# Performance work log

Measured on AMD Instinct MI355X. Metric: run time of the kernel, lower is better.

## Reference

```python
import jax, jax.numpy as jnp
import numpy as np

TAU = 0.7
N_NODES = 1024
N_EDGES = 32768

def _mlp3(x, W1, b1, W2, b2, W3, b3):
    h = jax.nn.relu(x @ W1 + b1)
    h = jax.nn.relu(h @ W2 + b2)
    return h @ W3 + b3

def _gcn_conv(x, src, dst, W, b, n):
    # PyG GCNConv(add_self_loops=False): out = D^-1/2 A D^-1/2 (x W) + b
    deg = jax.ops.segment_sum(jnp.ones(src.shape[0], x.dtype), dst, num_segments=n)
    dinv = jnp.where(deg > 0, jax.lax.rsqrt(jnp.maximum(deg, 1.0)), 0.0)
    h = x @ W
    msg = h[src] * (dinv[src] * dinv[dst])[:, None]
    return jax.ops.segment_sum(msg, dst, num_segments=n) + b

def _forward(x1, x11, x2, mlp_W1, mlp_b1, mlp_W2, mlp_b2, mlp_W3, mlp_b3,
             m1_W1, m1_b1, m1_W2, m1_b2, m1_W3, m1_b3,
             wm1, bp1, bp2, wm12, wm13, class2,
             gcn1_W, gcn1_b, wm2, gcn2_W, gcn2_b, fc_W, fc_b, src, dst):
    n = x1.shape[0]
    logits = _mlp3(x1, mlp_W1, mlp_b1, mlp_W2, mlp_b2, mlp_W3, mlp_b3)  # [N,3]
    g = _mlp3(x11, m1_W1, m1_b1, m1_W2, m1_b2, m1_W3, m1_b3)            # [N,2]
    # hard argmax routing, softened: tau at argmax, (1-tau)/2 at the 2 others
    oh = jax.nn.one_hot(jnp.argmax(logits, axis=1), 3, dtype=logits.dtype)
    r = oh * TAU + (1.0 - oh) * ((1.0 - TAU) * 0.5)                     # [N,3]
    # fused form of: (einsum('nj,jkl',g,class2) * x2[...,None]).sum(-1) + g@b1
    res1 = jnp.einsum('nj,jkl,nk->nk', g, class2, x2) + g @ bp1         # [N,768]
    # fused form of: (einsum('nj,jkl',r,wm1) * res1[...,None]).sum(-1) + r@b2
    res1 = jnp.einsum('nj,jkl,nk->nk', r, wm1, res1) + r @ bp2          # [N,768]
    h1 = jax.nn.relu(_gcn_conv(res1, src, dst, gcn1_W, gcn1_b, n))      # [N,256]
    h1 = (r @ wm12) * h1 + 2e-4 * (res1 @ wm13)                         # [N,256]
    res2 = jnp.einsum('nj,jkl,nk->nk', r, wm2, h1)                      # [N,256]
    h2 = jax.nn.relu(_gcn_conv(res2, src, dst, gcn2_W, gcn2_b, n))      # [N,32]
    return jax.nn.log_softmax(h2 @ fc_W + fc_b, axis=1)                 # [N,8]

def setup_inputs():
    key = jax.random.key(0)
    ks = jax.random.split(key, 32)
    f = jnp.float32
    nrm = lambda i, s, sc=0.05: sc * jax.random.normal(ks[i], s, f)
    return {
        'x1': nrm(0, (N_NODES, 768), 1.0),
        'x11': nrm(1, (N_NODES, 768), 1.0),
        'x2': nrm(2, (N_NODES, 768), 1.0),
        'mlp_W1': nrm(3, (768, 512)), 'mlp_b1': jnp.zeros((512,), f),
        'mlp_W2': nrm(4, (512, 512)), 'mlp_b2': jnp.zeros((512,), f),
        'mlp_W3': nrm(5, (512, 3)), 'mlp_b3': jnp.zeros((3,), f),
        'm1_W1': nrm(6, (768, 512)), 'm1_b1': jnp.zeros((512,), f),
        'm1_W2': nrm(7, (512, 512)), 'm1_b2': jnp.zeros((512,), f),
        'm1_W3': nrm(8, (512, 2)), 'm1_b3': jnp.zeros((2,), f),
        'wm1': nrm(9, (3, 768, 256)),
        'bp1': jnp.zeros((2, 768), f),
        'bp2': jnp.zeros((3, 768), f),
        'wm12': jnp.ones((3, 256), f),
        'wm13': nrm(10, (768, 256)),
        'class2': jnp.ones((2, 768, 64), f),
        'gcn1_W': nrm(11, (768, 256)), 'gcn1_b': jnp.zeros((256,), f),
        'wm2': nrm(12, (3, 256, 256)),
        'gcn2_W': nrm(13, (256, 32)), 'gcn2_b': jnp.zeros((32,), f),
        'fc_W': nrm(14, (32, 8)), 'fc_b': jnp.zeros((8,), f),
        'edge_index': jax.random.randint(ks[15], (2, N_EDGES), 0, N_NODES),
    }

def reference(x1, x11, x2, mlp_W1, mlp_b1, mlp_W2, mlp_b2, mlp_W3, mlp_b3,
              m1_W1, m1_b1, m1_W2, m1_b2, m1_W3, m1_b3,
              wm1, bp1, bp2, wm12, wm13, class2,
              gcn1_W, gcn1_b, wm2, gcn2_W, gcn2_b, fc_W, fc_b, edge_index):
    src, dst = edge_index[0], edge_index[1]
    return _forward(x1, x11, x2, mlp_W1, mlp_b1, mlp_W2, mlp_b2, mlp_W3, mlp_b3,
                    m1_W1, m1_b1, m1_W2, m1_b2, m1_W3, m1_b3,
                    wm1, bp1, bp2, wm12, wm13, class2,
                    gcn1_W, gcn1_b, wm2, gcn2_W, gcn2_b, fc_W, fc_b, src, dst)
```

## Files before the change

### kernel.cpp

```cpp
#include <hip/hip_runtime.h>
#include <hip/hip_bf16.h>

#define NN 1024
#define NE 32768
#define TAU 0.7f
#define GAPT 0.01f

typedef __attribute__((ext_vector_type(8))) short short8;
typedef __attribute__((ext_vector_type(4))) float f32x4;

__device__ inline ushort bf16rne(float x) {
    union { float f; unsigned u; } a; a.f = x;
    unsigned r = (a.u + 0x7FFFu + ((a.u >> 16) & 1u)) >> 16;
    return (ushort)r;
}
__device__ inline float bf16tof(ushort h) {
    union { unsigned u; float f; } a; a.u = ((unsigned)h) << 16;
    return a.f;
}
__device__ inline void bf16split(float x, ushort& h, ushort& l) {
    h = bf16rne(x);
    l = bf16rne(x - bf16tof(h));
}

template <int K, int EPI>
__device__ __forceinline__ void gemm_wave(
    int lane, int rt, int ct,
    const ushort* __restrict__ Ah, const ushort* __restrict__ Al,
    const ushort* __restrict__ Bh, const ushort* __restrict__ Bl,
    const float* __restrict__ bias, const float* __restrict__ W3,
    float* __restrict__ Cf, ushort* __restrict__ Oh, ushort* __restrict__ Ol, int N) {
    int r0 = rt * 16, c0 = ct * 32;
    int g = lane >> 4, q = lane & 15;
    const ushort* pah = Ah + (size_t)(r0 + q) * K + g * 8;
    const ushort* pal = Al + (size_t)(r0 + q) * K + g * 8;
    const ushort* pb0h = Bh + (size_t)(c0 + q) * K + g * 8;
    const ushort* pb0l = Bl + (size_t)(c0 + q) * K + g * 8;
    const ushort* pb1h = pb0h + (size_t)16 * K;
    const ushort* pb1l = pb0l + (size_t)16 * K;
    f32x4 acc0 = {0.f, 0.f, 0.f, 0.f};
    f32x4 acc1 = {0.f, 0.f, 0.f, 0.f};
#pragma unroll 2
    for (int k0 = 0; k0 < K; k0 += 32) {
        short8 ah = *(const short8*)(pah + k0);
        short8 al = *(const short8*)(pal + k0);
        short8 b0h = *(const short8*)(pb0h + k0);
        short8 b0l = *(const short8*)(pb0l + k0);
        short8 b1h = *(const short8*)(pb1h + k0);
        short8 b1l = *(const short8*)(pb1l + k0);
        acc0 = __builtin_amdgcn_mfma_f32_16x16x32_bf16(ah, b0h, acc0, 0, 0, 0);
        acc1 = __builtin_amdgcn_mfma_f32_16x16x32_bf16(ah, b1h, acc1, 0, 0, 0);
        acc0 = __builtin_amdgcn_mfma_f32_16x16x32_bf16(ah, b0l, acc0, 0, 0, 0);
        acc1 = __builtin_amdgcn_mfma_f32_16x16x32_bf16(ah, b1l, acc1, 0, 0, 0);
        acc0 = __builtin_amdgcn_mfma_f32_16x16x32_bf16(al, b0h, acc0, 0, 0, 0);
        acc1 = __builtin_amdgcn_mfma_f32_16x16x32_bf16(al, b1h, acc1, 0, 0, 0);
    }
    int col0 = c0 + q, col1 = c0 + 16 + q;
    if constexpr (EPI == 0) {
#pragma unroll
        for (int i = 0; i < 4; i++) {
            int row = r0 + g * 4 + i;
            Cf[(size_t)row * N + col0] = acc0[i];
            Cf[(size_t)row * N + col1] = acc1[i];
        }
    } else if constexpr (EPI == 1) {
        float bv0 = bias[col0], bv1 = bias[col1];
#pragma unroll
        for (int i = 0; i < 4; i++) {
            int row = r0 + g * 4 + i;
            float a0 = fmaxf(acc0[i] + bv0, 0.f);
            float a1 = fmaxf(acc1[i] + bv1, 0.f);
            ushort h, l;
            bf16split(a0, h, l);
            Oh[(size_t)row * N + col0] = h;
            Ol[(size_t)row * N + col0] = l;
            bf16split(a1, h, l);
            Oh[(size_t)row * N + col1] = h;
            Ol[(size_t)row * N + col1] = l;
        }
    } else {
        constexpr int J = (EPI == 2) ? 3 : 2;
        constexpr int STR = (EPI == 2) ? 4 : 2;
        float bv0 = bias[col0], bv1 = bias[col1];
        float s[4][J];
#pragma unroll
        for (int i = 0; i < 4; i++) {
            float a0 = fmaxf(acc0[i] + bv0, 0.f);
            float a1 = fmaxf(acc1[i] + bv1, 0.f);
#pragma unroll
            for (int j = 0; j < J; j++)
                s[i][j] = a0 * W3[col0 * J + j] + a1 * W3[col1 * J + j];
        }
#pragma unroll
        for (int i = 0; i < 4; i++)
#pragma unroll
            for (int j = 0; j < J; j++) {
                float v = s[i][j];
#pragma unroll
                for (int m = 1; m < 16; m <<= 1) v += __shfl_xor(v, m);
                s[i][j] = v;
            }
        if (q == 0) {
#pragma unroll
            for (int i = 0; i < 4; i++) {
                int row = r0 + g * 4 + i;
#pragma unroll
                for (int j = 0; j < J; j++) atomicAdd(&Cf[(size_t)row * STR + j], s[i][j]);
            }
        }
    }
}

template <int M, int N, int K, int EPI>
__global__ __launch_bounds__(256) void gemm3(
    const ushort* __restrict__ Ah, const ushort* __restrict__ Al,
    const ushort* __restrict__ Bh, const ushort* __restrict__ Bl,
    float* __restrict__ Cf) {
    constexpr int RT = M / 16;
    constexpr int JOBS = RT * (N / 32);
    int wid = (blockIdx.x * 256 + threadIdx.x) >> 6;
    if (wid >= JOBS) return;
    gemm_wave<K, EPI>(threadIdx.x & 63, wid % RT, wid / RT, Ah, Al, Bh, Bl,
                      nullptr, nullptr, Cf, nullptr, nullptr, N);
}

template <int K, int EPI0, int EPI1, int RIDER>
__global__ __launch_bounds__(256) void gemm_pair(
    const ushort* __restrict__ Ah0, const ushort* __restrict__ Al0,
    const ushort* __restrict__ Bh0, const ushort* __restrict__ Bl0,
    const float* __restrict__ bias0, const float* __restrict__ W30,
    float* __restrict__ Cf0, ushort* __restrict__ Oh0, ushort* __restrict__ Ol0,
    const ushort* __restrict__ Ah1, const ushort* __restrict__ Al1,
    const ushort* __restrict__ Bh1, const ushort* __restrict__ Bl1,
    const float* __restrict__ bias1, const float* __restrict__ W31,
    float* __restrict__ Cf1, ushort* __restrict__ Oh1, ushort* __restrict__ Ol1,
    const int* __restrict__ esrc, const int* __restrict__ edst,
    const int* __restrict__ deg, int* __restrict__ rowst, int* __restrict__ cursor,
    float* __restrict__ dinv, int* __restrict__ adj) {
    if (RIDER == 1 && blockIdx.x >= 512) {
        __shared__ int ps[256];
        int t = threadIdx.x;
        int4 d4 = *(const int4*)(deg + t * 4);
        int sum = d4.x + d4.y + d4.z + d4.w;
        ps[t] = sum;
        __syncthreads();
        for (int off = 1; off < 256; off <<= 1) {
            int v = (t >= off) ? ps[t - off] : 0;
            __syncthreads();
            ps[t] += v;
            __syncthreads();
        }
        int r0 = ps[t] - sum;
        int r1 = r0 + d4.x, r2 = r1 + d4.y, r3 = r2 + d4.z;
        rowst[t * 4 + 0] = r0;
        rowst[t * 4 + 1] = r1;
        rowst[t * 4 + 2] = r2;
        rowst[t * 4 + 3] = r3;
        if (t == 255) rowst[1024] = r3 + d4.w;
        cursor[t * 4 + 0] = r0;
        cursor[t * 4 + 1] = r1;
        cursor[t * 4 + 2] = r2;
        cursor[t * 4 + 3] = r3;
        dinv[t * 4 + 0] = d4.x > 0 ? rsqrtf((float)d4.x) : 0.f;
        dinv[t * 4 + 1] = d4.y > 0 ? rsqrtf((float)d4.y) : 0.f;
        dinv[t * 4 + 2] = d4.z > 0 ? rsqrtf((float)d4.z) : 0.f;
        dinv[t * 4 + 3] = d4.w > 0 ? rsqrtf((float)d4.w) : 0.f;
        return;
    }
    if (RIDER == 2 && blockIdx.x >= 512) {
        int e = (blockIdx.x - 512) * 256 + threadIdx.x;
        int d = edst[e];
        int slot = atomicAdd(&cursor[d], 1);
        adj[slot] = esrc[e];
        return;
    }
    int wid = (blockIdx.x * 256 + threadIdx.x) >> 6;
    int lane = threadIdx.x & 63;
    int pair = wid >> 10;
    int widl = wid & 1023;
    int rt = widl & 63, ct = widl >> 6;
    if (pair == 0)
        gemm_wave<K, EPI0>(lane, rt, ct, Ah0, Al0, Bh0, Bl0, bias0, W30, Cf0, Oh0, Ol0, 512);
    else
        gemm_wave<K, EPI1>(lane, rt, ct, Ah1, Al1, Bh1, Bl1, bias1, W31, Cf1, Oh1, Ol1, 512);
}

__device__ void dev_zero(int sub, int t, float* zbase) {
    for (int i = sub * 256 + t; i < 6144; i += 512) zbase[i] = 0.f;
}

__device__ void dev_tabs_wave(int gw, int lane, const float* __restrict__ class2,
                              const float* __restrict__ wm1, const float* __restrict__ wm2,
                              float* __restrict__ C2s, float* __restrict__ Wm1s,
                              float* __restrict__ Wm2s) {
    if (gw < 2304) {
        float4 v = *(const float4*)(wm1 + (size_t)gw * 256 + lane * 4);
        float s = v.x + v.y + v.z + v.w;
#pragma unroll
        for (int m = 32; m; m >>= 1) s += __shfl_xor(s, m);
        if (lane == 0) Wm1s[gw] = s;
    } else if (gw < 3072) {
        int j = gw - 2304;
        float4 v = *(const float4*)(wm2 + (size_t)j * 256 + lane * 4);
        float s = v.x + v.y + v.z + v.w;
#pragma unroll
        for (int m = 32; m; m >>= 1) s += __shfl_xor(s, m);
        if (lane == 0) Wm2s[j] = s;
    } else {
        int row = (gw - 3072) * 4 + (lane >> 4);
        float4 v = *(const float4*)(class2 + (size_t)row * 64 + (lane & 15) * 4);
        float s = v.x + v.y + v.z + v.w;
#pragma unroll
        for (int m = 8; m; m >>= 1) s += __shfl_xor(s, m);
        if ((lane & 15) == 0) C2s[row] = s;
    }
}

__device__ void dev_splitx(int sub, int t, const float* __restrict__ X,
                           ushort* __restrict__ Xh, ushort* __restrict__ Xl) {
    int j = sub * 256 + t;
    float4 v = ((const float4*)X)[j];
    ushort h0, l0, h1, l1, h2, l2, h3, l3;
    bf16split(v.x, h0, l0);
    bf16split(v.y, h1, l1);
    bf16split(v.z, h2, l2);
    bf16split(v.w, h3, l3);
    ((ushort4*)Xh)[j] = make_ushort4(h0, h1, h2, h3);
    ((ushort4*)Xl)[j] = make_ushort4(l0, l1, l2, l3);
}

__global__ __launch_bounds__(1024) void aux0(
    const float* class2, const float* wm1, const float* wm2,
    float* C2s, float* Wm1s, float* Wm2s, float* zbase,
    const float* x1, ushort* XH1, ushort* XL1,
    const float* x11, ushort* XH2, ushort* XL2,
    const float* W1a, ushort* W1AH, ushort* W1AL,
    const float* W1b, ushort* W1BH, ushort* W1BL,
    const float* W2a, ushort* W2AH, ushort* W2AL,
    const float* W2b, ushort* W2BH, ushort* W2BL,
    const float* G1W, ushort* GWH, ushort* GWL,
    const float* W13, const int* edst, int* deg) {
    __shared__ float tb[4][32][33];
    int quad = threadIdx.x >> 8;
    int t = threadIdx.x & 255;
    int sub = blockIdx.x * 4 + quad;
    if (sub >= 4194) return;
    const float* W = nullptr;
    ushort *Th = nullptr, *Tl = nullptr;
    int K = 0, N = 0, tile = 0;
    if (sub >= 4066) {
        int e = (sub - 4066) * 256 + t;
        atomicAdd(&deg[edst[e]], 1);
    }
    else if (sub >= 3874) { W = W13; Th = GWH + 256 * 768; Tl = GWL + 256 * 768; K = 768; N = 256; tile = sub - 3874; }
    else if (sub >= 3682) { W = G1W; Th = GWH; Tl = GWL; K = 768; N = 256; tile = sub - 3682; }
    else if (sub >= 3426) { W = W2b; Th = W2BH; Tl = W2BL; K = 512; N = 512; tile = sub - 3426; }
    else if (sub >= 3170) { W = W2a; Th = W2AH; Tl = W2AL; K = 512; N = 512; tile = sub - 3170; }
    else if (sub >= 2786) { W = W1b; Th = W1BH; Tl = W1BL; K = 768; N = 512; tile = sub - 2786; }
    else if (sub >= 2402) { W = W1a; Th = W1AH; Tl = W1AL; K = 768; N = 512; tile = sub - 2402; }
    int k0 = 0, n0 = 0;
    if (W) {
        k0 = (tile % (K / 32)) * 32;
        n0 = (tile / (K / 32)) * 32;
        int tx = t % 32, ty = t / 32;
        for (int i = ty; i < 32; i += 8)
            tb[quad][i][tx] = W[(size_t)(k0 + i) * N + n0 + tx];
    } else if (sub < 2) dev_zero(sub, t, zbase);
    else if (sub < 866) dev_tabs_wave((sub - 2) * 4 + (t >> 6), t & 63,
                                      class2, wm1, wm2, C2s, Wm1s, Wm2s);
    else if (sub < 1634) dev_splitx(sub - 866, t, x1, XH1, XL1);
    else if (sub < 2402) dev_splitx(sub - 1634, t, x11, XH2, XL2);
    __syncthreads();
    if (W) {
        int tx = t % 32, ty = t / 32;
        for (int i = ty; i < 32; i += 8) {
            float v = tb[quad][tx][i];
            ushort h, l;
            bf16split(v, h, l);
            Th[(size_t)(n0 + i) * K + k0 + tx] = h;
            Tl[(size_t)(n0 + i) * K + k0 + tx] = l;
        }
    }
}

__global__ __launch_bounds__(256) void finrep(
    const float* __restrict__ LG, const float* __restrict__ b3, float* __restrict__ rbuf,
    const float* __restrict__ x1, const float* __restrict__ W1, const float* __restrict__ b1,
    const float* __restrict__ W2, const float* __restrict__ b2, const float* __restrict__ W3) {
    __shared__ int snode[4];
    __shared__ int scnt;
    __shared__ float part[4][512];
    __shared__ float xs[768];
    __shared__ float h1[512];
    __shared__ float h2[512];
    int t = threadIdx.x;
    if (t == 0) scnt = 0;
    __syncthreads();
    if (t < 4) {
        int n = blockIdx.x * 4 + t;
        float l0 = LG[n * 4 + 0] + b3[0];
        float l1 = LG[n * 4 + 1] + b3[1];
        float l2 = LG[n * 4 + 2] + b3[2];
        int am = 0;
        float mv = l0;
        if (l1 > mv) { mv = l1; am = 1; }
        if (l2 > mv) { mv = l2; am = 2; }
        float sec = (am == 0) ? fmaxf(l1, l2) : ((am == 1) ? fmaxf(l0, l2) : fmaxf(l0, l1));
        float lo = (1.f - TAU) * 0.5f;
        rbuf[n * 4 + 0] = (am == 0) ? TAU : lo;
        rbuf[n * 4 + 1] = (am == 1) ? TAU : lo;
        rbuf[n * 4 + 2] = (am == 2) ? TAU : lo;
        if (mv - sec < GAPT) {
            int s = atomicAdd(&scnt, 1);
            snode[s] = n;
        }
    }
    __syncthreads();
    int cnt = scnt;
    int w = t >> 6, l = t & 63;
    for (int it = 0; it < cnt; it++) {
        int n = snode[it];
        for (int k = t; k < 768; k += 256) xs[k] = x1[(size_t)n * 768 + k];
        __syncthreads();
        {
            float acc[8] = {0.f, 0.f, 0.f, 0.f, 0.f, 0.f, 0.f, 0.f};
            for (int k = w * 192; k < (w + 1) * 192; k++) {
                float xv = xs[k];
                const float* wr = W1 + (size_t)k * 512 + l;
#pragma unroll
                for (int c = 0; c < 8; c++) acc[c] += xv * wr[64 * c];
            }
#pragma unroll
            for (int c = 0; c < 8; c++) part[w][l + 64 * c] = acc[c];
        }
        __syncthreads();
        for (int d = t; d < 512; d += 256)
            h1[d] = fmaxf(part[0][d] + part[1][d] + part[2][d] + part[3][d] + b1[d], 0.f);
        __syncthreads();
        {
            float acc[8] = {0.f, 0.f, 0.f, 0.f, 0.f, 0.f, 0.f, 0.f};
            for (int k = w * 128; k < (w + 1) * 128; k++) {
                float xv = h1[k];
                const float* wr = W2 + (size_t)k * 512 + l;
#pragma unroll
                for (int c = 0; c < 8; c++) acc[c] += xv * wr[64 * c];
            }
#pragma unroll
            for (int c = 0; c < 8; c++) part[w][l + 64 * c] = acc[c];
        }
        __syncthreads();
        for (int d = t; d < 512; d += 256)
            h2[d] = fmaxf(part[0][d] + part[1][d] + part[2][d] + part[3][d] + b2[d], 0.f);
        __syncthreads();
        if (t < 64) {
            float p0 = 0.f, p1 = 0.f, p2 = 0.f;
            for (int k = t; k < 512; k += 64) {
                float hv = h2[k];
                p0 += hv * W3[k * 3 + 0];
                p1 += hv * W3[k * 3 + 1];
                p2 += hv * W3[k * 3 + 2];
            }
            for (int off = 32; off; off >>= 1) {
                p0 += __shfl_down(p0, off);
                p1 += __shfl_down(p1, off);
                p2 += __shfl_down(p2, off);
            }
            if (t == 0) {
                float l0 = p0 + b3[0], l1 = p1 + b3[1], l2 = p2 + b3[2];
                int am = 0;
                float mv = l0;
                if (l1 > mv) { mv = l1; am = 1; }
                if (l2 > mv) { mv = l2; am = 2; }
                float lo = (1.f - TAU) * 0.5f;
                rbuf[n * 4 + 0] = (am == 0) ? TAU : lo;
                rbuf[n * 4 + 1] = (am == 1) ? TAU : lo;
                rbuf[n * 4 + 2] = (am == 2) ? TAU : lo;
            }
        }
        __syncthreads();
    }
}

__global__ __launch_bounds__(256) void res1_kernel(
    const float* __restrict__ x2, const float* __restrict__ G, const float* __restrict__ m1b3,
    const float* __restrict__ rbuf, const float* __restrict__ C2s, const float* __restrict__ bp1,
    const float* __restrict__ Wm1s, const float* __restrict__ bp2,
    ushort* __restrict__ r1h, ushort* __restrict__ r1l) {
    int idx = blockIdx.x * 256 + threadIdx.x;
    int n = idx / 192;
    int kq = (idx % 192) * 4;
    float g0 = G[n * 2 + 0] + m1b3[0], g1 = G[n * 2 + 1] + m1b3[1];
    float r0 = rbuf[n * 4 + 0], r1 = rbuf[n * 4 + 1], r2 = rbuf[n * 4 + 2];
    float4 xv = *(const float4*)(x2 + (size_t)n * 768 + kq);
    float4 c0 = *(const float4*)(C2s + kq);
    float4 c1 = *(const float4*)(C2s + 768 + kq);
    float4 p0 = *(const float4*)(bp1 + kq);
    float4 p1 = *(const float4*)(bp1 + 768 + kq);
    float4 w0 = *(const float4*)(Wm1s + kq);
    float4 w1 = *(const float4*)(Wm1s + 768 + kq);
    float4 w2 = *(const float4*)(Wm1s + 1536 + kq);
    float4 q0 = *(const float4*)(bp2 + kq);
    float4 q1 = *(const float4*)(bp2 + 768 + kq);
    float4 q2 = *(const float4*)(bp2 + 1536 + kq);
    float o[4];
    o[0] = (xv.x * (g0 * c0.x + g1 * c1.x) + g0 * p0.x + g1 * p1.x) * (r0 * w0.x + r1 * w1.x + r2 * w2.x) + r0 * q0.x + r1 * q1.x + r2 * q2.x;
    o[1] = (xv.y * (g0 * c0.y + g1 * c1.y) + g0 * p0.y + g1 * p1.y) * (r0 * w0.y + r1 * w1.y + r2 * w2.y) + r0 * q0.y + r1 * q1.y + r2 * q2.y;
    o[2] = (xv.z * (g0 * c0.z + g1 * c1.z) + g0 * p0.z + g1 * p1.z) * (r0 * w0.z + r1 * w1.z + r2 * w2.z) + r0 * q0.z + r1 * q1.z + r2 * q2.z;
    o[3] = (xv.w * (g0 * c0.w + g1 * c1.w) + g0 * p0.w + g1 * p1.w) * (r0 * w0.w + r1 * w1.w + r2 * w2.w) + r0 * q0.w + r1 * q1.w + r2 * q2.w;
    ushort h[4], l[4];
#pragma unroll
    for (int i = 0; i < 4; i++) bf16split(o[i], h[i], l[i]);
    size_t off = ((size_t)n * 768 + kq) / 4;
    ((ushort4*)r1h)[off] = make_ushort4(h[0], h[1], h[2], h[3]);
    ((ushort4*)r1l)[off] = make_ushort4(l[0], l[1], l[2], l[3]);
}

__global__ __launch_bounds__(256) void gather1_combine(
    const float* __restrict__ gcw, const int* __restrict__ rowst, const int* __restrict__ adj,
    const float* __restrict__ dinv, const float* __restrict__ gcn1_b,
    const float* __restrict__ rbuf, const float* __restrict__ wm12,
    const float* __restrict__ Wm2s, float* __restrict__ res2f) {
    int n = blockIdx.x;
    int k = threadIdx.x;
    int lane = threadIdx.x & 63;
    int e0 = rowst[n], e1 = rowst[n + 1];
    float acc = 0.f;
    for (int base = e0; base < e1; base += 64) {
        int idx = base + lane;
        int s_i = 0;
        float w_i = 0.f;
        if (idx < e1) { s_i = adj[idx]; w_i = dinv[s_i]; }
        int mm = min(64, e1 - base);
        for (int j = 0; j < mm; j++) {
            int s = __shfl(s_i, j);
            float w = __shfl(w_i, j);
            acc += gcw[(size_t)s * 512 + k] * w;
        }
    }
    float h1 = dinv[n] * acc + gcn1_b[k];
    float mv = gcw[(size_t)n * 512 + 256 + k];
    float r0 = rbuf[n * 4 + 0], r1 = rbuf[n * 4 + 1], r2 = rbuf[n * 4 + 2];
    float a = r0 * wm12[k] + r1 * wm12[256 + k] + r2 * wm12[512 + k];
    float w = r0 * Wm2s[k] + r1 * Wm2s[256 + k] + r2 * Wm2s[512 + k];
    res2f[(size_t)n * 256 + k] = w * (a * fmaxf(h1, 0.f) + 2e-4f * mv);
}

__global__ __launch_bounds__(256) void gather2_full(
    const float* __restrict__ res2f, const int* __restrict__ rowst,
    const int* __restrict__ adj, const float* __restrict__ dinv,
    const float* __restrict__ G2W, const float* __restrict__ gcn2_b,
    const float* __restrict__ fcW, const float* __restrict__ fcb,
    float* __restrict__ out) {
    __shared__ float gres[256];
    __shared__ float part[8][32];
    int t = threadIdx.x;
    int lane = t & 63;
    int n = blockIdx.x;
    int e0 = rowst[n], e1 = rowst[n + 1];
    float acc = 0.f;
    for (int base = e0; base < e1; base += 64) {
        int idx = base + lane;
        int s_i = 0;
        float w_i = 0.f;
        if (idx < e1) { s_i = adj[idx]; w_i = dinv[s_i]; }
        int mm = min(64, e1 - base);
        for (int j = 0; j < mm; j++) {
            int s = __shfl(s_i, j);
            float w = __shfl(w_i, j);
            acc += res2f[(size_t)s * 256 + t] * w;
        }
    }
    gres[t] = acc * dinv[n];
    __syncthreads();
    int j = t & 31, seg = t >> 5;
    float p = 0.f;
#pragma unroll
    for (int kk = 0; kk < 32; kk++) {
        int k = seg * 32 + kk;
        p += gres[k] * G2W[k * 32 + j];
    }
    part[seg][j] = p;
    __syncthreads();
    if (t < 32) {
        float h2 = part[0][t] + part[1][t] + part[2][t] + part[3][t] +
                   part[4][t] + part[5][t] + part[6][t] + part[7][t] + gcn2_b[t];
        gres[t] = fmaxf(h2, 0.f);
    }
    __syncthreads();
    if (t < 8) {
        float logit = fcb[t];
#pragma unroll
        for (int i = 0; i < 32; i++) logit += gres[i] * fcW[i * 8 + t];
        float m = logit;
        for (int off = 4; off; off >>= 1) m = fmaxf(m, __shfl_xor(m, off, 8));
        float e = expf(logit - m), s = e;
        for (int off = 4; off; off >>= 1) s += __shfl_xor(s, off, 8);
        out[(size_t)n * 8 + t] = logit - m - logf(s);
    }
}

extern "C" void kernel_launch(void* const* d_in, const int* in_sizes, int n_in,
                              void* d_out, int out_size, void* d_ws, size_t ws_size,
                              hipStream_t stream) {
    const float* x1     = (const float*)d_in[0];
    const float* x11    = (const float*)d_in[1];
    const float* x2     = (const float*)d_in[2];
    const float* mlp_W1 = (const float*)d_in[3];
    const float* mlp_b1 = (const float*)d_in[4];
    const float* mlp_W2 = (const float*)d_in[5];
    const float* mlp_b2 = (const float*)d_in[6];
    const float* mlp_W3 = (const float*)d_in[7];
    const float* mlp_b3 = (const float*)d_in[8];
    const float* m1_W1  = (const float*)d_in[9];
    const float* m1_b1  = (const float*)d_in[10];
    const float* m1_W2  = (const float*)d_in[11];
    const float* m1_b2  = (const float*)d_in[12];
    const float* m1_W3  = (const float*)d_in[13];
    const float* m1_b3  = (const float*)d_in[14];
    const float* wm1    = (const float*)d_in[15];
    const float* bp1    = (const float*)d_in[16];
    const float* bp2    = (const float*)d_in[17];
    const float* wm12   = (const float*)d_in[18];
    const float* wm13   = (const float*)d_in[19];
    const float* class2 = (const float*)d_in[20];
    const float* gcn1_W = (const float*)d_in[21];
    const float* gcn1_b = (const float*)d_in[22];
    const float* wm2    = (const float*)d_in[23];
    const float* gcn2_W = (const float*)d_in[24];
    const float* gcn2_b = (const float*)d_in[25];
    const float* fc_W   = (const float*)d_in[26];
    const float* fc_b   = (const float*)d_in[27];
    const int* eidx     = (const int*)d_in[28];
    const int* esrc = eidx;
    const int* edst = eidx + NE;

    char* ws = (char*)d_ws;
    ushort* XH1   = (ushort*)(ws + 0x0000000);
    ushort* XL1   = (ushort*)(ws + 0x0180000);
    ushort* XH2   = (ushort*)(ws + 0x0300000);
    ushort* XL2   = (ushort*)(ws + 0x0480000);
    ushort* W1AH  = (ushort*)(ws + 0x0600000);
    ushort* W1AL  = (ushort*)(ws + 0x06C0000);
    ushort* W1BH  = (ushort*)(ws + 0x0780000);
    ushort* W1BL  = (ushort*)(ws + 0x0840000);
    ushort* W2AH  = (ushort*)(ws + 0x0900000);
    ushort* W2AL  = (ushort*)(ws + 0x0980000);
    ushort* W2BH  = (ushort*)(ws + 0x0A00000);
    ushort* W2BL  = (ushort*)(ws + 0x0A80000);
    ushort* GWH   = (ushort*)(ws + 0x0B00000);
    ushort* GWL   = (ushort*)(ws + 0x0BC0000);
    ushort* HS1AH = (ushort*)(ws + 0x0D00000);
    ushort* HS1AL = (ushort*)(ws + 0x0E00000);
    ushort* HS1BH = (ushort*)(ws + 0x0F00000);
    ushort* HS1BL = (ushort*)(ws + 0x1000000);
    ushort* RES1H = (ushort*)(ws + 0x1100000);
    ushort* RES1L = (ushort*)(ws + 0x1280000);
    float*  GCW   = (float*)(ws + 0x1400000);
    float*  RES2F = (float*)(ws + 0x1600000);
    float* LOGITS = (float*)(ws + 0x1740000);
    float* GBUF   = (float*)(ws + 0x1744000);
    float* RBUF   = (float*)(ws + 0x1746000);
    float* DINV   = (float*)(ws + 0x174A000);
    int*   ROWST  = (int*)(ws + 0x174B000);
    int*   CURS   = (int*)(ws + 0x174D000);
    int*   ADJ    = (int*)(ws + 0x174E000);
    int*   DEG    = (int*)(ws + 0x176E000);
    float* C2S    = (float*)(ws + 0x1770000);
    float* WM1S   = (float*)(ws + 0x1772000);
    float* WM2S   = (float*)(ws + 0x1775000);

    hipMemsetAsync(DEG, 0, NN * sizeof(int), stream);
    aux0<<<1049, 1024, 0, stream>>>(class2, wm1, wm2, C2S, WM1S, WM2S, LOGITS,
                                    x1, XH1, XL1, x11, XH2, XL2,
                                    mlp_W1, W1AH, W1AL, m1_W1, W1BH, W1BL,
                                    mlp_W2, W2AH, W2AL, m1_W2, W2BH, W2BL,
                                    gcn1_W, GWH, GWL, wm13, edst, DEG);
    gemm_pair<768, 1, 1, 1><<<513, 256, 0, stream>>>(
        XH1, XL1, W1AH, W1AL, mlp_b1, nullptr, nullptr, HS1AH, HS1AL,
        XH2, XL2, W1BH, W1BL, m1_b1, nullptr, nullptr, HS1BH, HS1BL,
        esrc, edst, DEG, ROWST, CURS, DINV, ADJ);
    gemm_pair<512, 2, 3, 2><<<640, 256, 0, stream>>>(
        HS1AH, HS1AL, W2AH, W2AL, mlp_b2, mlp_W3, LOGITS, nullptr, nullptr,
        HS1BH, HS1BL, W2BH, W2BL, m1_b2, m1_W3, GBUF, nullptr, nullptr,
        esrc, edst, DEG, ROWST, CURS, DINV, ADJ);
    finrep<<<256, 256, 0, stream>>>(LOGITS, mlp_b3, RBUF, x1, mlp_W1, mlp_b1,
                                    mlp_W2, mlp_b2, mlp_W3);
    res1_kernel<<<768, 256, 0, stream>>>(x2, GBUF, m1_b3, RBUF, C2S, bp1, WM1S, bp2,
                                         RES1H, RES1L);
    gemm3<1024, 512, 768, 0><<<256, 256, 0, stream>>>(RES1H, RES1L, GWH, GWL, GCW);
    gather1_combine<<<NN, 256, 0, stream>>>(GCW, ROWST, ADJ, DINV, gcn1_b, RBUF,
                                            wm12, WM2S, RES2F);
    gather2_full<<<NN, 256, 0, stream>>>(RES2F, ROWST, ADJ, DINV, gcn2_W, gcn2_b,
                                         fc_W, fc_b, (float*)d_out);
}
```

Measured before the change: 170.2 us.

## Replace global degree atomics with per-block LDS histograms and split GCN GEMM finer

```diff
diff --git a/kernel.cpp b/kernel.cpp
--- a/kernel.cpp
+++ b/kernel.cpp
@@ -111,17 +111,40 @@
     }
 }
 
-template <int M, int N, int K, int EPI>
-__global__ __launch_bounds__(256) void gemm3(
+template <int M, int N, int K>
+__global__ __launch_bounds__(256) void gemm3_n16(
     const ushort* __restrict__ Ah, const ushort* __restrict__ Al,
     const ushort* __restrict__ Bh, const ushort* __restrict__ Bl,
     float* __restrict__ Cf) {
     constexpr int RT = M / 16;
-    constexpr int JOBS = RT * (N / 32);
+    constexpr int JOBS = RT * (N / 16);
     int wid = (blockIdx.x * 256 + threadIdx.x) >> 6;
     if (wid >= JOBS) return;
-    gemm_wave<K, EPI>(threadIdx.x & 63, wid % RT, wid / RT, Ah, Al, Bh, Bl,
-                      nullptr, nullptr, Cf, nullptr, nullptr, N);
+    int lane = threadIdx.x & 63;
+    int rt = wid % RT, ct = wid / RT;
+    int r0 = rt * 16, c0 = ct * 16;
+    int g = lane >> 4, q = lane & 15;
+    const ushort* pah = Ah + (size_t)(r0 + q) * K + g * 8;
+    const ushort* pal = Al + (size_t)(r0 + q) * K + g * 8;
+    const ushort* pbh = Bh + (size_t)(c0 + q) * K + g * 8;
+    const ushort* pbl = Bl + (size_t)(c0 + q) * K + g * 8;
+    f32x4 acc = {0.f, 0.f, 0.f, 0.f};
+#pragma unroll 2
+    for (int k0 = 0; k0 < K; k0 += 32) {
+        short8 ah = *(const short8*)(pah + k0);
+        short8 al = *(const short8*)(pal + k0);
+        short8 bh = *(const short8*)(pbh + k0);
+        short8 bl = *(const short8*)(pbl + k0);
+        acc = __builtin_amdgcn_mfma_f32_16x16x32_bf16(ah, bh, acc, 0, 0, 0);
+        acc = __builtin_amdgcn_mfma_f32_16x16x32_bf16(ah, bl, acc, 0, 0, 0);
+        acc = __builtin_amdgcn_mfma_f32_16x16x32_bf16(al, bh, acc, 0, 0, 0);
+    }
+    int col = c0 + q;
+#pragma unroll
+    for (int i = 0; i < 4; i++) {
+        int row = r0 + g * 4 + i;
+        Cf[(size_t)row * N + col] = acc[i];
+    }
 }
 
 template <int K, int EPI0, int EPI1, int RIDER>
@@ -135,13 +158,18 @@
     const float* __restrict__ bias1, const float* __restrict__ W31,
     float* __restrict__ Cf1, ushort* __restrict__ Oh1, ushort* __restrict__ Ol1,
     const int* __restrict__ esrc, const int* __restrict__ edst,
-    const int* __restrict__ deg, int* __restrict__ rowst, int* __restrict__ cursor,
+    const int* __restrict__ part, int* __restrict__ rowst, int* __restrict__ cursor,
     float* __restrict__ dinv, int* __restrict__ adj) {
     if (RIDER == 1 && blockIdx.x >= 512) {
         __shared__ int ps[256];
         int t = threadIdx.x;
-        int4 d4 = *(const int4*)(deg + t * 4);
-        int sum = d4.x + d4.y + d4.z + d4.w;
+        int d0 = 0, d1 = 0, d2 = 0, d3 = 0;
+#pragma unroll
+        for (int b = 0; b < 8; b++) {
+            int4 qv = *(const int4*)(part + b * 1024 + t * 4);
+            d0 += qv.x; d1 += qv.y; d2 += qv.z; d3 += qv.w;
+        }
+        int sum = d0 + d1 + d2 + d3;
         ps[t] = sum;
         __syncthreads();
         for (int off = 1; off < 256; off <<= 1) {
@@ -151,20 +179,20 @@
             __syncthreads();
         }
         int r0 = ps[t] - sum;
-        int r1 = r0 + d4.x, r2 = r1 + d4.y, r3 = r2 + d4.z;
+        int r1 = r0 + d0, r2 = r1 + d1, r3 = r2 + d2;
         rowst[t * 4 + 0] = r0;
         rowst[t * 4 + 1] = r1;
         rowst[t * 4 + 2] = r2;
         rowst[t * 4 + 3] = r3;
-        if (t == 255) rowst[1024] = r3 + d4.w;
+        if (t == 255) rowst[1024] = r3 + d3;
         cursor[t * 4 + 0] = r0;
         cursor[t * 4 + 1] = r1;
         cursor[t * 4 + 2] = r2;
         cursor[t * 4 + 3] = r3;
-        dinv[t * 4 + 0] = d4.x > 0 ? rsqrtf((float)d4.x) : 0.f;
-        dinv[t * 4 + 1] = d4.y > 0 ? rsqrtf((float)d4.y) : 0.f;
-        dinv[t * 4 + 2] = d4.z > 0 ? rsqrtf((float)d4.z) : 0.f;
-        dinv[t * 4 + 3] = d4.w > 0 ? rsqrtf((float)d4.w) : 0.f;
+        dinv[t * 4 + 0] = d0 > 0 ? rsqrtf((float)d0) : 0.f;
+        dinv[t * 4 + 1] = d1 > 0 ? rsqrtf((float)d1) : 0.f;
+        dinv[t * 4 + 2] = d2 > 0 ? rsqrtf((float)d2) : 0.f;
+        dinv[t * 4 + 3] = d3 > 0 ? rsqrtf((float)d3) : 0.f;
         return;
     }
     if (RIDER == 2 && blockIdx.x >= 512) {
@@ -239,20 +267,29 @@
     const float* W2a, ushort* W2AH, ushort* W2AL,
     const float* W2b, ushort* W2BH, ushort* W2BL,
     const float* G1W, ushort* GWH, ushort* GWL,
-    const float* W13, const int* edst, int* deg) {
+    const float* W13, const int* edst, int* part) {
+    if (blockIdx.x >= 1017) {
+        __shared__ int hist[1024];
+        int b = blockIdx.x - 1017;
+        int t = threadIdx.x;
+        hist[t] = 0;
+        __syncthreads();
+        const int* ep = edst + b * 4096;
+#pragma unroll
+        for (int i = 0; i < 4; i++) atomicAdd(&hist[ep[t + i * 1024]], 1);
+        __syncthreads();
+        part[b * 1024 + t] = hist[t];
+        return;
+    }
     __shared__ float tb[4][32][33];
     int quad = threadIdx.x >> 8;
     int t = threadIdx.x & 255;
     int sub = blockIdx.x * 4 + quad;
-    if (sub >= 4194) return;
+    if (sub >= 4066) return;
     const float* W = nullptr;
     ushort *Th = nullptr, *Tl = nullptr;
     int K = 0, N = 0, tile = 0;
-    if (sub >= 4066) {
-        int e = (sub - 4066) * 256 + t;
-        atomicAdd(&deg[edst[e]], 1);
-    }
-    else if (sub >= 3874) { W = W13; Th = GWH + 256 * 768; Tl = GWL + 256 * 768; K = 768; N = 256; tile = sub - 3874; }
+    if (sub >= 3874)      { W = W13; Th = GWH + 256 * 768; Tl = GWL + 256 * 768; K = 768; N = 256; tile = sub - 3874; }
     else if (sub >= 3682) { W = G1W; Th = GWH; Tl = GWL; K = 768; N = 256; tile = sub - 3682; }
     else if (sub >= 3426) { W = W2b; Th = W2BH; Tl = W2BL; K = 512; N = 512; tile = sub - 3426; }
     else if (sub >= 3170) { W = W2a; Th = W2AH; Tl = W2AL; K = 512; N = 512; tile = sub - 3170; }
@@ -269,7 +306,7 @@
     else if (sub < 866) dev_tabs_wave((sub - 2) * 4 + (t >> 6), t & 63,
                                       class2, wm1, wm2, C2s, Wm1s, Wm2s);
     else if (sub < 1634) dev_splitx(sub - 866, t, x1, XH1, XL1);
-    else if (sub < 2402) dev_splitx(sub - 1634, t, x11, XH2, XL2);
+    else dev_splitx(sub - 1634, t, x11, XH2, XL2);
     __syncthreads();
     if (W) {
         int tx = t % 32, ty = t / 32;
@@ -564,30 +601,29 @@
     int*   ROWST  = (int*)(ws + 0x174B000);
     int*   CURS   = (int*)(ws + 0x174D000);
     int*   ADJ    = (int*)(ws + 0x174E000);
-    int*   DEG    = (int*)(ws + 0x176E000);
+    int*   PART   = (int*)(ws + 0x1780000);
     float* C2S    = (float*)(ws + 0x1770000);
     float* WM1S   = (float*)(ws + 0x1772000);
     float* WM2S   = (float*)(ws + 0x1775000);
 
-    hipMemsetAsync(DEG, 0, NN * sizeof(int), stream);
-    aux0<<<1049, 1024, 0, stream>>>(class2, wm1, wm2, C2S, WM1S, WM2S, LOGITS,
+    aux0<<<1025, 1024, 0, stream>>>(class2, wm1, wm2, C2S, WM1S, WM2S, LOGITS,
                                     x1, XH1, XL1, x11, XH2, XL2,
                                     mlp_W1, W1AH, W1AL, m1_W1, W1BH, W1BL,
                                     mlp_W2, W2AH, W2AL, m1_W2, W2BH, W2BL,
-                                    gcn1_W, GWH, GWL, wm13, edst, DEG);
+                                    gcn1_W, GWH, GWL, wm13, edst, PART);
     gemm_pair<768, 1, 1, 1><<<513, 256, 0, stream>>>(
         XH1, XL1, W1AH, W1AL, mlp_b1, nullptr, nullptr, HS1AH, HS1AL,
         XH2, XL2, W1BH, W1BL, m1_b1, nullptr, nullptr, HS1BH, HS1BL,
-        esrc, edst, DEG, ROWST, CURS, DINV, ADJ);
+        esrc, edst, PART, ROWST, CURS, DINV, ADJ);
     gemm_pair<512, 2, 3, 2><<<640, 256, 0, stream>>>(
         HS1AH, HS1AL, W2AH, W2AL, mlp_b2, mlp_W3, LOGITS, nullptr, nullptr,
         HS1BH, HS1BL, W2BH, W2BL, m1_b2, m1_W3, GBUF, nullptr, nullptr,
-        esrc, edst, DEG, ROWST, CURS, DINV, ADJ);
+        esrc, edst, PART, ROWST, CURS, DINV, ADJ);
     finrep<<<256, 256, 0, stream>>>(LOGITS, mlp_b3, RBUF, x1, mlp_W1, mlp_b1,
                                     mlp_W2, mlp_b2, mlp_W3);
     res1_kernel<<<768, 256, 0, stream>>>(x2, GBUF, m1_b3, RBUF, C2S, bp1, WM1S, bp2,
                                          RES1H, RES1L);
-    gemm3<1024, 512, 768, 0><<<256, 256, 0, stream>>>(RES1H, RES1L, GWH, GWL, GCW);
+    gemm3_n16<1024, 512, 768><<<512, 256, 0, stream>>>(RES1H, RES1L, GWH, GWL, GCW);
     gather1_combine<<<NN, 256, 0, stream>>>(GCW, ROWST, ADJ, DINV, gcn1_b, RBUF,
                                             wm12, WM2S, RES2F);
     gather2_full<<<NN, 256, 0, stream>>>(RES2F, ROWST, ADJ, DINV, gcn2_W, gcn2_b,
```

Result: faster. 165.4 us (-2.8%).
